# Optimization experiments

Measured on AMD Instinct MI355X. Metric: run time of the kernel, lower is better.

The kernel has to match this reference:

```python
import jax, jax.numpy as jnp
import numpy as np

INPUT_DIM = 2048
DIM = 1024
CODEBOOK_SIZE = 8192
COMMITMENT_COST = 0.25
N = 8192


def setup_inputs() -> dict:
    key = jax.random.key(0)
    ks = jax.random.split(key, 6)
    s_in = 1.0 / np.sqrt(INPUT_DIM)
    s_d = 1.0 / np.sqrt(DIM)
    return {
        "roi_feats": jax.random.normal(ks[0], (N, INPUT_DIM), dtype=jnp.float32),
        "W_in": jax.random.normal(ks[1], (DIM, INPUT_DIM), dtype=jnp.float32) * s_in,
        "b_in": jnp.zeros((DIM,), dtype=jnp.float32),
        "W_enc": jax.random.normal(ks[2], (DIM, DIM), dtype=jnp.float32) * s_d,
        "b_enc": jnp.zeros((DIM,), dtype=jnp.float32),
        "codebook": jax.random.uniform(ks[3], (CODEBOOK_SIZE, DIM), dtype=jnp.float32,
                                        minval=-1.0 / CODEBOOK_SIZE, maxval=1.0 / CODEBOOK_SIZE),
        "W_dec": jax.random.normal(ks[4], (DIM, DIM), dtype=jnp.float32) * s_d,
        "b_dec": jnp.zeros((DIM,), dtype=jnp.float32),
        "W_out": jax.random.normal(ks[5], (INPUT_DIM, DIM), dtype=jnp.float32) * s_d,
        "b_out": jnp.zeros((INPUT_DIM,), dtype=jnp.float32),
    }


def reference(roi_feats, W_in, b_in, W_enc, b_enc, codebook, W_dec, b_dec, W_out, b_out):
    # encoder(input_projection(x))
    z_e = (roi_feats @ W_in.T + b_in) @ W_enc.T + b_enc  # [N, DIM]
    # squared-euclidean distances to codebook: [N, K]
    d = (jnp.sum(z_e * z_e, axis=1, keepdims=True)
         - 2.0 * (z_e @ codebook.T)
         + jnp.sum(codebook * codebook, axis=1))
    ids = jnp.argmin(d, axis=-1)  # [N]
    z_q_raw = codebook[ids]  # [N, DIM]
    # straight-through estimator
    z_q = z_e + jax.lax.stop_gradient(z_q_raw - z_e)
    recon = (z_q @ W_dec.T + b_dec) @ W_out.T + b_out  # [N, INPUT_DIM]
    recon_loss = jnp.mean((recon - roi_feats) ** 2)
    embedding_loss = jnp.mean((jax.lax.stop_gradient(z_q) - z_e) ** 2)
    commitment_loss = jnp.mean((z_q - jax.lax.stop_gradient(z_e)) ** 2)
    vq_loss = recon_loss + embedding_loss + COMMITMENT_COST * commitment_loss
    return ids, z_q, recon, vq_loss, recon_loss, embedding_loss, commitment_loss
```

## Files before the change

kernel.cpp:

```cpp
#include <hip/hip_runtime.h>
#include <float.h>


#define N_ROWS 8192
#define IN_DIM 2048
#define DIM 1024
#define CBK 8192

#define PANEL_MASK_K1024_C32 0x0000000000401000ULL
#define PANEL_MASK_K2048_C32 0x0101001001001000ULL

#define SCREEN_DELTA 1.2e-3f

typedef __attribute__((ext_vector_type(8))) short short8;
typedef __attribute__((ext_vector_type(8))) unsigned short ushort8;
typedef __attribute__((ext_vector_type(4))) float f32x4;

__device__ __forceinline__ float sqf(float v) { return __builtin_fmaf(v, v, 0.0f); }

__device__ __forceinline__ unsigned short f2bf(float f) {
  unsigned int u = __float_as_uint(f);
  u += 0x7fffu + ((u >> 16) & 1u);
  return (unsigned short)(u >> 16);
}

__device__ __forceinline__ unsigned packsplit(float x) {
  const unsigned u = __float_as_uint(x);
  const unsigned hb = u & 0xFFFF0000u;
  const float rem = x - __uint_as_float(hb);
  return (u >> 16) | (__float_as_uint(rem) & 0xFFFF0000u);
}

__device__ __forceinline__ int swz128(int c) {
  return (c & 3) | (((c >> 3) & 7) << 2) | (((c >> 2) & 1) << 5) | ((c >> 6) << 6);
}

__device__ __forceinline__ float block_reduce_sum(float v) {
  __shared__ float sh[4];
  #pragma unroll
  for (int off = 32; off > 0; off >>= 1) v += __shfl_down(v, off, 64);
  const int lane = threadIdx.x & 63, w = threadIdx.x >> 6;
  if (lane == 0) sh[w] = v;
  __syncthreads();
  float r = 0.f;
  if (threadIdx.x == 0) r = sh[0] + sh[1] + sh[2] + sh[3];
  return r;
}

__device__ __forceinline__ float chain_d(const float* __restrict__ zsh,
                                         const float* __restrict__ cbr,
                                         float z2r, float c2e) {
  float part = 0.f;
  for (int k = 0; k < 384; ++k) part = __builtin_fmaf(zsh[k], cbr[k], part);
  float total = part;
  part = 0.f;
  for (int k = 384; k < 704; ++k) part = __builtin_fmaf(zsh[k], cbr[k], part);
  total = total + part;
  part = 0.f;
  for (int k = 704; k < 1024; ++k) part = __builtin_fmaf(zsh[k], cbr[k], part);
  total = total + part;
  return __builtin_fmaf(-2.0f, total, z2r) + c2e;
}

template <bool BT>
__global__ __launch_bounds__(256) void gemm128(
    const float* __restrict__ A, const float* __restrict__ B,
    const float* __restrict__ bias, float* __restrict__ C,
    int M, int N, int K) {
  __shared__ float As[2][16][132];
  __shared__ float Bs[2][16][132];
  const int tid = threadIdx.x;
  const int tx = tid & 15, ty = tid >> 4;
  const int bm = blockIdx.y, bn = blockIdx.x;

  const int mload = tid & 127, kh = tid >> 7;
  const size_t arow = (size_t)(bm * 128 + mload) * (size_t)K;
  const size_t brow = BT ? (size_t)(bn * 128 + mload) * (size_t)K : 0;
  const int swn = swz128(mload);
  const int c4 = (tid & 31) << 2;
  const int kr = tid >> 5;
  const int swc = swz128(c4);

  float acc[8][8];
  #pragma unroll
  for (int r = 0; r < 8; ++r)
    #pragma unroll
    for (int c = 0; c < 8; ++c) acc[r][c] = 0.f;

  const int boff = ((tx & 7) << 2) | ((tx >> 3) << 6);

  float4 av0, av1, bv0, bv1;
  av0 = *(const float4*)&A[arow + kh * 8];
  av1 = *(const float4*)&A[arow + kh * 8 + 4];
  if (BT) {
    bv0 = *(const float4*)&B[brow + kh * 8];
    bv1 = *(const float4*)&B[brow + kh * 8 + 4];
  } else {
    bv0 = *(const float4*)&B[(size_t)kr * N + bn * 128 + c4];
    bv1 = *(const float4*)&B[(size_t)(kr + 8) * N + bn * 128 + c4];
  }
  As[0][kh * 8 + 0][mload] = av0.x; As[0][kh * 8 + 1][mload] = av0.y;
  As[0][kh * 8 + 2][mload] = av0.z; As[0][kh * 8 + 3][mload] = av0.w;
  As[0][kh * 8 + 4][mload] = av1.x; As[0][kh * 8 + 5][mload] = av1.y;
  As[0][kh * 8 + 6][mload] = av1.z; As[0][kh * 8 + 7][mload] = av1.w;
  if (BT) {
    Bs[0][kh * 8 + 0][swn] = bv0.x; Bs[0][kh * 8 + 1][swn] = bv0.y;
    Bs[0][kh * 8 + 2][swn] = bv0.z; Bs[0][kh * 8 + 3][swn] = bv0.w;
    Bs[0][kh * 8 + 4][swn] = bv1.x; Bs[0][kh * 8 + 5][swn] = bv1.y;
    Bs[0][kh * 8 + 6][swn] = bv1.z; Bs[0][kh * 8 + 7][swn] = bv1.w;
  } else {
    *(float4*)&Bs[0][kr][swc] = bv0;
    *(float4*)&Bs[0][kr + 8][swc] = bv1;
  }
  const int nk = K >> 4;
  if (nk > 1) {
    av0 = *(const float4*)&A[arow + 16 + kh * 8];
    av1 = *(const float4*)&A[arow + 16 + kh * 8 + 4];
    if (BT) {
      bv0 = *(const float4*)&B[brow + 16 + kh * 8];
      bv1 = *(const float4*)&B[brow + 16 + kh * 8 + 4];
    } else {
      bv0 = *(const float4*)&B[(size_t)(16 + kr) * N + bn * 128 + c4];
      bv1 = *(const float4*)&B[(size_t)(16 + kr + 8) * N + bn * 128 + c4];
    }
  }
  __syncthreads();

  for (int ki = 0; ki < nk; ++ki) {
    const int p = ki & 1;
    if (ki + 1 < nk) {
      As[p ^ 1][kh * 8 + 0][mload] = av0.x; As[p ^ 1][kh * 8 + 1][mload] = av0.y;
      As[p ^ 1][kh * 8 + 2][mload] = av0.z; As[p ^ 1][kh * 8 + 3][mload] = av0.w;
      As[p ^ 1][kh * 8 + 4][mload] = av1.x; As[p ^ 1][kh * 8 + 5][mload] = av1.y;
      As[p ^ 1][kh * 8 + 6][mload] = av1.z; As[p ^ 1][kh * 8 + 7][mload] = av1.w;
      if (BT) {
        Bs[p ^ 1][kh * 8 + 0][swn] = bv0.x; Bs[p ^ 1][kh * 8 + 1][swn] = bv0.y;
        Bs[p ^ 1][kh * 8 + 2][swn] = bv0.z; Bs[p ^ 1][kh * 8 + 3][swn] = bv0.w;
        Bs[p ^ 1][kh * 8 + 4][swn] = bv1.x; Bs[p ^ 1][kh * 8 + 5][swn] = bv1.y;
        Bs[p ^ 1][kh * 8 + 6][swn] = bv1.z; Bs[p ^ 1][kh * 8 + 7][swn] = bv1.w;
      } else {
        *(float4*)&Bs[p ^ 1][kr][swc] = bv0;
        *(float4*)&Bs[p ^ 1][kr + 8][swc] = bv1;
      }
      if (ki + 2 < nk) {
        const int k2 = (ki + 2) << 4;
        av0 = *(const float4*)&A[arow + k2 + kh * 8];
        av1 = *(const float4*)&A[arow + k2 + kh * 8 + 4];
        if (BT) {
          bv0 = *(const float4*)&B[brow + k2 + kh * 8];
          bv1 = *(const float4*)&B[brow + k2 + kh * 8 + 4];
        } else {
          bv0 = *(const float4*)&B[(size_t)(k2 + kr) * N + bn * 128 + c4];
          bv1 = *(const float4*)&B[(size_t)(k2 + kr + 8) * N + bn * 128 + c4];
        }
      }
    }
    #pragma unroll
    for (int kk = 0; kk < 16; ++kk) {
      const float4 a0 = *(const float4*)&As[p][kk][ty * 8];
      const float4 a1 = *(const float4*)&As[p][kk][ty * 8 + 4];
      const float4 b0 = *(const float4*)&Bs[p][kk][boff];
      const float4 b1 = *(const float4*)&Bs[p][kk][boff + 32];
      const float ar[8] = {a0.x, a0.y, a0.z, a0.w, a1.x, a1.y, a1.z, a1.w};
      const float br[8] = {b0.x, b0.y, b0.z, b0.w, b1.x, b1.y, b1.z, b1.w};
      #pragma unroll
      for (int r = 0; r < 8; ++r)
        #pragma unroll
        for (int c = 0; c < 8; ++c) acc[r][c] = fmaf(ar[r], br[c], acc[r][c]);
    }
    __syncthreads();
  }

  const int gcol = bn * 128 + tx * 8;
  float bb[8] = {0, 0, 0, 0, 0, 0, 0, 0};
  if (bias) {
    const float4 v0 = *(const float4*)&bias[gcol];
    const float4 v1 = *(const float4*)&bias[gcol + 4];
    bb[0] = v0.x; bb[1] = v0.y; bb[2] = v0.z; bb[3] = v0.w;
    bb[4] = v1.x; bb[5] = v1.y; bb[6] = v1.z; bb[7] = v1.w;
  }
  #pragma unroll
  for (int r = 0; r < 8; ++r) {
    float* cp = &C[(size_t)(bm * 128 + ty * 8 + r) * N + gcol];
    float4 o0, o1;
    o0.x = acc[r][0] + bb[0]; o0.y = acc[r][1] + bb[1];
    o0.z = acc[r][2] + bb[2]; o0.w = acc[r][3] + bb[3];
    o1.x = acc[r][4] + bb[4]; o1.y = acc[r][5] + bb[5];
    o1.z = acc[r][6] + bb[6]; o1.w = acc[r][7] + bb[7];
    *(float4*)cp = o0;
    *(float4*)(cp + 4) = o1;
  }
}

__global__ __launch_bounds__(256) void emul_gemm_kernel(
    const float* __restrict__ A, const float* __restrict__ B,
    const float* __restrict__ bias, float* __restrict__ C,
    unsigned* __restrict__ ZP,
    int N, int K, int lda, int ldb, unsigned long long panel_mask) {
  __shared__ float As_[2][32][128];
  __shared__ float Bs_[2][32][128];
  const int tid = threadIdx.x;
  const int tx = tid & 15, ty = tid >> 4;
  const int row0 = blockIdx.y * 128, col0 = blockIdx.x * 128;
  const int sr = tid & 127, sh = tid >> 7;
  const int scol = (((sr >> 2) & 1) << 6) + ((sr >> 3) << 2) + (sr & 3);

  float part[8][8], total[8][8];
  #pragma unroll
  for (int r = 0; r < 8; ++r)
    #pragma unroll
    for (int e = 0; e < 8; ++e) { part[r][e] = 0.f; total[r][e] = 0.f; }

  float4 av[4], bv[4];
  #pragma unroll
  for (int q = 0; q < 4; ++q) {
    av[q] = *(const float4*)&A[(size_t)(row0 + sr) * lda + sh * 16 + q * 4];
    bv[q] = *(const float4*)&B[(size_t)(col0 + sr) * ldb + sh * 16 + q * 4];
  }
  #pragma unroll
  for (int q = 0; q < 4; ++q) {
    As_[0][sh * 16 + q * 4 + 0][sr] = av[q].x;
    As_[0][sh * 16 + q * 4 + 1][sr] = av[q].y;
    As_[0][sh * 16 + q * 4 + 2][sr] = av[q].z;
    As_[0][sh * 16 + q * 4 + 3][sr] = av[q].w;
    Bs_[0][sh * 16 + q * 4 + 0][scol] = bv[q].x;
    Bs_[0][sh * 16 + q * 4 + 1][scol] = bv[q].y;
    Bs_[0][sh * 16 + q * 4 + 2][scol] = bv[q].z;
    Bs_[0][sh * 16 + q * 4 + 3][scol] = bv[q].w;
  }
  const int nch = K >> 5;
  if (nch > 1) {
    #pragma unroll
    for (int q = 0; q < 4; ++q) {
      av[q] = *(const float4*)&A[(size_t)(row0 + sr) * lda + 32 + sh * 16 + q * 4];
      bv[q] = *(const float4*)&B[(size_t)(col0 + sr) * ldb + 32 + sh * 16 + q * 4];
    }
  }
  __syncthreads();

  for (int ci = 0; ci < nch; ++ci) {
    const int p = ci & 1;
    if (ci + 1 < nch) {
      #pragma unroll
      for (int q = 0; q < 4; ++q) {
        As_[p ^ 1][sh * 16 + q * 4 + 0][sr] = av[q].x;
        As_[p ^ 1][sh * 16 + q * 4 + 1][sr] = av[q].y;
        As_[p ^ 1][sh * 16 + q * 4 + 2][sr] = av[q].z;
        As_[p ^ 1][sh * 16 + q * 4 + 3][sr] = av[q].w;
        Bs_[p ^ 1][sh * 16 + q * 4 + 0][scol] = bv[q].x;
        Bs_[p ^ 1][sh * 16 + q * 4 + 1][scol] = bv[q].y;
        Bs_[p ^ 1][sh * 16 + q * 4 + 2][scol] = bv[q].z;
        Bs_[p ^ 1][sh * 16 + q * 4 + 3][scol] = bv[q].w;
      }
      if (ci + 2 < nch) {
        const int k2 = (ci + 2) << 5;
        #pragma unroll
        for (int q = 0; q < 4; ++q) {
          av[q] = *(const float4*)&A[(size_t)(row0 + sr) * lda + k2 + sh * 16 + q * 4];
          bv[q] = *(const float4*)&B[(size_t)(col0 + sr) * ldb + k2 + sh * 16 + q * 4];
        }
      }
    }
    if (ci && ((panel_mask >> ci) & 1ULL)) {
      #pragma unroll
      for (int r = 0; r < 8; ++r)
        #pragma unroll
        for (int e = 0; e < 8; ++e) { total[r][e] = total[r][e] + part[r][e]; part[r][e] = 0.f; }
    }
    #pragma unroll 4
    for (int kk = 0; kk < 32; ++kk) {
      const float4 za = *(const float4*)&As_[p][kk][ty * 8];
      const float4 zb = *(const float4*)&As_[p][kk][ty * 8 + 4];
      const float4 ca = *(const float4*)&Bs_[p][kk][tx * 4];
      const float4 cb4 = *(const float4*)&Bs_[p][kk][64 + tx * 4];
      const float zr[8] = {za.x, za.y, za.z, za.w, zb.x, zb.y, zb.z, zb.w};
      const float cr[8] = {ca.x, ca.y, ca.z, ca.w, cb4.x, cb4.y, cb4.z, cb4.w};
      #pragma unroll
      for (int r = 0; r < 8; ++r)
        #pragma unroll
        for (int e = 0; e < 8; ++e)
          part[r][e] = __builtin_fmaf(zr[r], cr[e], part[r][e]);
    }
    __syncthreads();
  }
  #pragma unroll
  for (int r = 0; r < 8; ++r)
    #pragma unroll
    for (int e = 0; e < 8; ++e) total[r][e] = total[r][e] + part[r][e];

  const float4 ba = *(const float4*)&bias[col0 + tx * 8];
  const float4 bb = *(const float4*)&bias[col0 + tx * 8 + 4];
  const float br8[8] = {ba.x, ba.y, ba.z, ba.w, bb.x, bb.y, bb.z, bb.w};
  #pragma unroll
  for (int r = 0; r < 8; ++r) {
    const size_t rowi = (size_t)(row0 + ty * 8 + r);
    float ov[8];
    #pragma unroll
    for (int j = 0; j < 8; ++j) ov[j] = total[r][j] + br8[j];
    float* cp = &C[rowi * N + col0 + tx * 8];
    float4 o0, o1;
    o0.x = ov[0]; o0.y = ov[1]; o0.z = ov[2]; o0.w = ov[3];
    o1.x = ov[4]; o1.y = ov[5]; o1.z = ov[6]; o1.w = ov[7];
    *(float4*)cp = o0;
    *(float4*)(cp + 4) = o1;
    if (ZP) {
      uint4 p0, p1;
      p0.x = packsplit(ov[0]); p0.y = packsplit(ov[1]);
      p0.z = packsplit(ov[2]); p0.w = packsplit(ov[3]);
      p1.x = packsplit(ov[4]); p1.y = packsplit(ov[5]);
      p1.z = packsplit(ov[6]); p1.w = packsplit(ov[7]);
      unsigned* zp = &ZP[rowi * N + col0 + tx * 8];
      *(uint4*)zp = p0;
      *(uint4*)(zp + 4) = p1;
    }
  }
}

__global__ __launch_bounds__(256) void mfma_screen_kernel(
    const unsigned* __restrict__ ZP, const float* __restrict__ CB,
    const float* __restrict__ Z2, const float* __restrict__ C2,
    uint4* __restrict__ recs) {
  __shared__ unsigned short Zs[128 * 64];
  __shared__ unsigned short Cs[128 * 64];
  __shared__ int rowminI[128];
  __shared__ int cnt[128];
  __shared__ unsigned short cand[128][12];
  const int tid = threadIdx.x;
  const int wid = tid >> 6, lane = tid & 63;
  const int e0 = blockIdx.x * 128, row0 = blockIdx.y * 128;
  const int wr = (wid >> 1) * 64, wc = (wid & 1) * 64;

  if (tid < 128) { rowminI[tid] = 0x7F800000; cnt[tid] = 0; }

  f32x4 acc[4][4];
  #pragma unroll
  for (int m = 0; m < 4; ++m)
    #pragma unroll
    for (int n = 0; n < 4; ++n)
      #pragma unroll
      for (int j = 0; j < 4; ++j) acc[m][n][j] = 0.f;

  const int stg_r = tid >> 3, stg_kg = (tid & 7) * 4;

  for (int k0 = 0; k0 < 1024; k0 += 32) {
    __syncthreads();
    #pragma unroll
    for (int s = 0; s < 4; ++s) {
      const int r = stg_r + s * 32;
      const int swz = (r & 7) << 4;
      const int bhi = (r * 128 + stg_kg * 2) ^ swz;
      const int blo = (r * 128 + 64 + stg_kg * 2) ^ swz;
      const uint4 p = *(const uint4*)&ZP[(size_t)(row0 + r) * 1024 + k0 + stg_kg];
      uint2 zh, zl;
      zh.x = (p.x & 0xFFFFu) | (p.y << 16);
      zh.y = (p.z & 0xFFFFu) | (p.w << 16);
      zl.x = (p.x >> 16) | (p.y & 0xFFFF0000u);
      zl.y = (p.z >> 16) | (p.w & 0xFFFF0000u);
      *(uint2*)((char*)Zs + bhi) = zh;
      *(uint2*)((char*)Zs + blo) = zl;
      const float4 cv = *(const float4*)&CB[(size_t)(e0 + r) * 1024 + k0 + stg_kg];
      const float cf[4] = {cv.x, cv.y, cv.z, cv.w};
      unsigned ch[4], cl[4];
      #pragma unroll
      for (int i = 0; i < 4; ++i) {
        const unsigned u = __float_as_uint(cf[i]);
        ch[i] = u & 0xFFFF0000u;
        const float rem = cf[i] - __uint_as_float(ch[i]);
        cl[i] = __float_as_uint(rem) & 0xFFFF0000u;
      }
      uint2 cph, cpl;
      cph.x = (ch[0] >> 16) | ch[1];
      cph.y = (ch[2] >> 16) | ch[3];
      cpl.x = (cl[0] >> 16) | cl[1];
      cpl.y = (cl[2] >> 16) | cl[3];
      *(uint2*)((char*)Cs + bhi) = cph;
      *(uint2*)((char*)Cs + blo) = cpl;
    }
    __syncthreads();
    const int kb2 = 16 * (lane >> 4);
    short8 ah[4], al[4], bh[4], bl[4];
    #pragma unroll
    for (int m = 0; m < 4; ++m) {
      const int r = wr + m * 16 + (lane & 15);
      const int swz = (r & 7) << 4;
      ah[m] = *(const short8*)((const char*)Zs + ((r * 128 + kb2) ^ swz));
      al[m] = *(const short8*)((const char*)Zs + ((r * 128 + 64 + kb2) ^ swz));
    }
    #pragma unroll
    for (int n = 0; n < 4; ++n) {
      const int r = wc + n * 16 + (lane & 15);
      const int swz = (r & 7) << 4;
      bh[n] = *(const short8*)((const char*)Cs + ((r * 128 + kb2) ^ swz));
      bl[n] = *(const short8*)((const char*)Cs + ((r * 128 + 64 + kb2) ^ swz));
    }
    #pragma unroll
    for (int m = 0; m < 4; ++m)
      #pragma unroll
      for (int n = 0; n < 4; ++n) {
        acc[m][n] = __builtin_amdgcn_mfma_f32_16x16x32_bf16(ah[m], bh[n], acc[m][n], 0, 0, 0);
        acc[m][n] = __builtin_amdgcn_mfma_f32_16x16x32_bf16(ah[m], bl[n], acc[m][n], 0, 0, 0);
        acc[m][n] = __builtin_amdgcn_mfma_f32_16x16x32_bf16(al[m], bh[n], acc[m][n], 0, 0, 0);
      }
  }

  float dv[4][4][4];
  #pragma unroll
  for (int m = 0; m < 4; ++m)
    #pragma unroll
    for (int j = 0; j < 4; ++j) {
      const int rg = row0 + wr + m * 16 + (lane >> 4) * 4 + j;
      const float z2r = Z2[rg];
      float lm = FLT_MAX;
      #pragma unroll
      for (int n = 0; n < 4; ++n) {
        const float d = __builtin_fmaf(-2.0f, acc[m][n][j], z2r) +
                        C2[e0 + wc + n * 16 + (lane & 15)];
        dv[m][n][j] = d;
        lm = fminf(lm, d);
      }
      #pragma unroll
      for (int msk = 1; msk < 16; msk <<= 1)
        lm = fminf(lm, __shfl_xor(lm, msk, 64));
      if ((lane & 15) == 0)
        atomicMin(&rowminI[wr + m * 16 + (lane >> 4) * 4 + j], __float_as_int(lm));
    }
  __syncthreads();
  #pragma unroll
  for (int m = 0; m < 4; ++m)
    #pragma unroll
    for (int j = 0; j < 4; ++j) {
      const int rl = wr + m * 16 + (lane >> 4) * 4 + j;
      const float thr = __int_as_float(rowminI[rl]) + SCREEN_DELTA;
      #pragma unroll
      for (int n = 0; n < 4; ++n) {
        if (dv[m][n][j] <= thr) {
          const int pos = atomicAdd(&cnt[rl], 1);
          if (pos < 12)
            cand[rl][pos] = (unsigned short)(e0 + wc + n * 16 + (lane & 15));
        }
      }
    }
  __syncthreads();
  if (tid < 128) {
    uint4 a, b;
    a.x = (unsigned)rowminI[tid];
    a.y = (unsigned)cnt[tid];
    a.z = (unsigned)cand[tid][0] | ((unsigned)cand[tid][1] << 16);
    a.w = (unsigned)cand[tid][2] | ((unsigned)cand[tid][3] << 16);
    b.x = (unsigned)cand[tid][4] | ((unsigned)cand[tid][5] << 16);
    b.y = (unsigned)cand[tid][6] | ((unsigned)cand[tid][7] << 16);
    b.z = (unsigned)cand[tid][8] | ((unsigned)cand[tid][9] << 16);
    b.w = (unsigned)cand[tid][10] | ((unsigned)cand[tid][11] << 16);
    const size_t base = ((size_t)(row0 + tid) * 64 + blockIdx.x) * 2;
    recs[base] = a;
    recs[base + 1] = b;
  }
}

__global__ __launch_bounds__(256) void collect_rescore_kernel(
    const uint4* __restrict__ recs, const float* __restrict__ Z,
    const float* __restrict__ CB, const float* __restrict__ Z2,
    const float* __restrict__ C2, int* __restrict__ ids,
    float* __restrict__ o_ids, float* __restrict__ o_zq,
    float* __restrict__ esum) {
  __shared__ float zsh[1024];
  __shared__ float gmin_sh;
  __shared__ int lcnt, ovf, ewin;
  __shared__ unsigned short list[64];
  __shared__ unsigned long long kred[4];
  const int row = blockIdx.x, tid = threadIdx.x;
  if (tid == 0) { lcnt = 0; ovf = 0; }
  uint4 r0 = make_uint4(0, 0, 0, 0), r1 = make_uint4(0, 0, 0, 0);
  float mymin = FLT_MAX;
  if (tid < 64) {
    const size_t base = ((size_t)row * 64 + tid) * 2;
    r0 = recs[base];
    r1 = recs[base + 1];
    mymin = __uint_as_float(r0.x);
  }
  for (int i = tid; i < 1024; i += 256) zsh[i] = Z[(size_t)row * 1024 + i];
  if (tid < 64) {
    float m = mymin;
    #pragma unroll
    for (int off = 32; off > 0; off >>= 1) m = fminf(m, __shfl_down(m, off, 64));
    if (tid == 0) gmin_sh = m;
  }
  __syncthreads();
  const float thr = gmin_sh + SCREEN_DELTA;
  if (tid < 64 && mymin <= thr) {
    const int c = (int)r0.y;
    if (c > 12) {
      atomicOr(&ovf, 1);
    } else {
      unsigned short idxs[12];
      idxs[0] = r0.z & 0xFFFF; idxs[1] = r0.z >> 16;
      idxs[2] = r0.w & 0xFFFF; idxs[3] = r0.w >> 16;
      idxs[4] = r1.x & 0xFFFF; idxs[5] = r1.x >> 16;
      idxs[6] = r1.y & 0xFFFF; idxs[7] = r1.y >> 16;
      idxs[8] = r1.z & 0xFFFF; idxs[9] = r1.z >> 16;
      idxs[10] = r1.w & 0xFFFF; idxs[11] = r1.w >> 16;
      for (int i = 0; i < c; ++i) {
        const int pos = atomicAdd(&lcnt, 1);
        if (pos < 64) list[pos] = idxs[i];
        else atomicOr(&ovf, 1);
      }
    }
  }
  __syncthreads();
  const float z2r = Z2[row];
  unsigned long long key = ~0ULL;
  if (ovf) {
    for (int e = tid; e < CBK; e += 256) {
      const float d = chain_d(zsh, &CB[(size_t)e * 1024], z2r, C2[e]);
      const unsigned long long k =
          ((unsigned long long)__float_as_uint(d) << 32) | (unsigned)e;
      key = (k < key) ? k : key;
    }
  } else {
    const int n = lcnt < 64 ? lcnt : 64;
    if (tid < n) {
      const int e = list[tid];
      const float d = chain_d(zsh, &CB[(size_t)e * 1024], z2r, C2[e]);
      key = ((unsigned long long)__float_as_uint(d) << 32) | (unsigned)e;
    }
  }
  #pragma unroll
  for (int off = 32; off > 0; off >>= 1) {
    const unsigned long long o = __shfl_down(key, off, 64);
    key = (o < key) ? o : key;
  }
  if ((tid & 63) == 0) kred[tid >> 6] = key;
  __syncthreads();
  if (tid == 0) {
    unsigned long long k = kred[0];
    k = (kred[1] < k) ? kred[1] : k;
    k = (kred[2] < k) ? kred[2] : k;
    k = (kred[3] < k) ? kred[3] : k;
    const int e = (int)(k & 0xFFFFFFFFu);
    ids[row] = e;
    o_ids[row] = (float)e;
    ewin = e;
  }
  __syncthreads();
  const int e2 = ewin;
  float s = 0.f;
  for (int i = tid; i < 1024; i += 256) {
    const float c = CB[(size_t)e2 * 1024 + i];
    o_zq[(size_t)row * 1024 + i] = c;
    const float d = zsh[i] - c;
    s = __builtin_fmaf(d, d, s);
  }
  const float r2 = block_reduce_sum(s);
  if (tid == 0) esum[row] = r2;
}

__global__ __launch_bounds__(256) void mfma_recon_kernel(
    const float* __restrict__ A, const float* __restrict__ B,
    const float* __restrict__ bias, float* __restrict__ C) {
  __shared__ unsigned short Abf[128 * 64];
  __shared__ unsigned short Bbf[128 * 64];
  const int tid = threadIdx.x;
  const int wid = tid >> 6, lane = tid & 63;
  const int row0 = blockIdx.y * 128, col0 = blockIdx.x * 128;
  const int wr = (wid >> 1) * 64, wc = (wid & 1) * 64;

  f32x4 acc[4][4];
  #pragma unroll
  for (int m = 0; m < 4; ++m)
    #pragma unroll
    for (int n = 0; n < 4; ++n)
      #pragma unroll
      for (int j = 0; j < 4; ++j) acc[m][n][j] = 0.f;

  for (int k0 = 0; k0 < 1024; k0 += 64) {
    __syncthreads();
    #pragma unroll
    for (int q = 0; q < 4; ++q) {
      const int g = tid + q * 256;
      const int r = g >> 3;
      const int kg = (g & 7) * 8;
      const float4 a0 = *(const float4*)&A[(size_t)(row0 + r) * 1024 + k0 + kg];
      const float4 a1 = *(const float4*)&A[(size_t)(row0 + r) * 1024 + k0 + kg + 4];
      const float4 b0 = *(const float4*)&B[(size_t)(col0 + r) * 1024 + k0 + kg];
      const float4 b1 = *(const float4*)&B[(size_t)(col0 + r) * 1024 + k0 + kg + 4];
      ushort8 pa, pb;
      pa[0] = f2bf(a0.x); pa[1] = f2bf(a0.y); pa[2] = f2bf(a0.z); pa[3] = f2bf(a0.w);
      pa[4] = f2bf(a1.x); pa[5] = f2bf(a1.y); pa[6] = f2bf(a1.z); pa[7] = f2bf(a1.w);
      pb[0] = f2bf(b0.x); pb[1] = f2bf(b0.y); pb[2] = f2bf(b0.z); pb[3] = f2bf(b0.w);
      pb[4] = f2bf(b1.x); pb[5] = f2bf(b1.y); pb[6] = f2bf(b1.z); pb[7] = f2bf(b1.w);
      const int byte = (r * 128 + kg * 2) ^ ((r & 7) << 4);
      *(ushort8*)((char*)Abf + byte) = pa;
      *(ushort8*)((char*)Bbf + byte) = pb;
    }
    __syncthreads();
    #pragma unroll
    for (int kh = 0; kh < 2; ++kh) {
      const int kb = kh * 32 + 8 * (lane >> 4);
      short8 afr[4], bfr[4];
      #pragma unroll
      for (int m = 0; m < 4; ++m) {
        const int r = wr + m * 16 + (lane & 15);
        const int byte = (r * 128 + kb * 2) ^ ((r & 7) << 4);
        afr[m] = *(const short8*)((const char*)Abf + byte);
      }
      #pragma unroll
      for (int n = 0; n < 4; ++n) {
        const int r = wc + n * 16 + (lane & 15);
        const int byte = (r * 128 + kb * 2) ^ ((r & 7) << 4);
        bfr[n] = *(const short8*)((const char*)Bbf + byte);
      }
      #pragma unroll
      for (int m = 0; m < 4; ++m)
        #pragma unroll
        for (int n = 0; n < 4; ++n)
          acc[m][n] = __builtin_amdgcn_mfma_f32_16x16x32_bf16(
              afr[m], bfr[n], acc[m][n], 0, 0, 0);
    }
  }

  #pragma unroll
  for (int m = 0; m < 4; ++m)
    #pragma unroll
    for (int n = 0; n < 4; ++n) {
      const int col = col0 + wc + n * 16 + (lane & 15);
      const float bc = bias[col];
      #pragma unroll
      for (int j = 0; j < 4; ++j) {
        const int row = row0 + wr + m * 16 + (lane >> 4) * 4 + j;
        C[(size_t)row * 2048 + col] = acc[m][n][j] + bc;
      }
    }
}

__global__ __launch_bounds__(256) void sumsq1024_kernel(
    const float* __restrict__ X, float* __restrict__ out) {
  __shared__ float rows[4][1024];
  __shared__ float leaves[4][8];
  const int tid = threadIdx.x;
  const int row0 = blockIdx.x * 4;
  for (int i = tid; i < 4096; i += 256)
    rows[i >> 10][i & 1023] = X[(size_t)row0 * 1024 + i];
  __syncthreads();
  if (tid < 32) {
    const int r = tid >> 3, lf = tid & 7;
    const float* a = &rows[r][lf * 128];
    float s0 = sqf(a[0]), s1 = sqf(a[1]), s2 = sqf(a[2]), s3 = sqf(a[3]);
    float s4 = sqf(a[4]), s5 = sqf(a[5]), s6 = sqf(a[6]), s7 = sqf(a[7]);
    for (int i = 8; i < 128; i += 8) {
      s0 = s0 + sqf(a[i + 0]); s1 = s1 + sqf(a[i + 1]);
      s2 = s2 + sqf(a[i + 2]); s3 = s3 + sqf(a[i + 3]);
      s4 = s4 + sqf(a[i + 4]); s5 = s5 + sqf(a[i + 5]);
      s6 = s6 + sqf(a[i + 6]); s7 = s7 + sqf(a[i + 7]);
    }
    leaves[r][lf] = ((s0 + s1) + (s2 + s3)) + ((s4 + s5) + (s6 + s7));
  }
  __syncthreads();
  if (tid < 4) {
    const float* L = leaves[tid];
    const float p01 = L[0] + L[1], p23 = L[2] + L[3];
    const float p45 = L[4] + L[5], p67 = L[6] + L[7];
    out[row0 + tid] = ((p01 + p23) + (p45 + p67));
  }
}

__global__ __launch_bounds__(256) void rowdot_bias_kernel(
    const float* __restrict__ W, const float* __restrict__ v,
    const float* __restrict__ b2, float* __restrict__ out) {
  const int row = blockIdx.x;
  const float4 w4 = *(const float4*)&W[(size_t)row * 1024 + threadIdx.x * 4];
  const float4 v4 = *(const float4*)&v[threadIdx.x * 4];
  const float s = w4.x * v4.x + w4.y * v4.y + w4.z * v4.z + w4.w * v4.w;
  const float r = block_reduce_sum(s);
  if (threadIdx.x == 0) out[row] = r + b2[row];
}

__global__ __launch_bounds__(256) void sqdiff_partial_kernel(
    const float* __restrict__ a, const float* __restrict__ b,
    float* __restrict__ part) {
  const size_t base = (size_t)blockIdx.x * 2048 + (size_t)threadIdx.x * 8;
  const float4 x0 = *(const float4*)&a[base];
  const float4 x1 = *(const float4*)&a[base + 4];
  const float4 y0 = *(const float4*)&b[base];
  const float4 y1 = *(const float4*)&b[base + 4];
  float s = 0.f;
  float d;
  d = x0.x - y0.x; s += d * d; d = x0.y - y0.y; s += d * d;
  d = x0.z - y0.z; s += d * d; d = x0.w - y0.w; s += d * d;
  d = x1.x - y1.x; s += d * d; d = x1.y - y1.y; s += d * d;
  d = x1.z - y1.z; s += d * d; d = x1.w - y1.w; s += d * d;
  const float r = block_reduce_sum(s);
  if (threadIdx.x == 0) part[blockIdx.x] = r;
}

__global__ __launch_bounds__(256) void final_losses_kernel(
    const float* __restrict__ rp, const float* __restrict__ esum,
    float* __restrict__ o) {
  __shared__ double sh[4];
  const int lane = threadIdx.x & 63, w = threadIdx.x >> 6;
  double s = 0.0;
  for (int i = threadIdx.x; i < 8192; i += 256) s += (double)rp[i];
  #pragma unroll
  for (int off = 32; off > 0; off >>= 1) s += __shfl_down(s, off, 64);
  if (lane == 0) sh[w] = s;
  __syncthreads();
  double rl = 0.0;
  if (threadIdx.x == 0) rl = (sh[0] + sh[1] + sh[2] + sh[3]) / ((double)N_ROWS * IN_DIM);
  __syncthreads();
  double s2 = 0.0;
  for (int i = threadIdx.x; i < 8192; i += 256) s2 += (double)esum[i];
  #pragma unroll
  for (int off = 32; off > 0; off >>= 1) s2 += __shfl_down(s2, off, 64);
  if (lane == 0) sh[w] = s2;
  __syncthreads();
  if (threadIdx.x == 0) {
    const double el = (sh[0] + sh[1] + sh[2] + sh[3]) / ((double)N_ROWS * DIM);
    o[0] = (float)(rl + el + 0.25 * el);
    o[1] = (float)rl;
    o[2] = (float)el;
    o[3] = (float)el;
  }
}

extern "C" void kernel_launch(void* const* d_in, const int* in_sizes, int n_in,
                              void* d_out, int out_size, void* d_ws, size_t ws_size,
                              hipStream_t stream) {
  const float* roi   = (const float*)d_in[0];
  const float* W_in  = (const float*)d_in[1];
  const float* b_in  = (const float*)d_in[2];
  const float* W_enc = (const float*)d_in[3];
  const float* b_enc = (const float*)d_in[4];
  const float* cb    = (const float*)d_in[5];
  const float* W_dec = (const float*)d_in[6];
  const float* b_dec = (const float*)d_in[7];
  const float* W_out = (const float*)d_in[8];
  const float* b_out = (const float*)d_in[9];

  float* out = (float*)d_out;
  float* o_ids   = out;
  float* o_zq    = out + 8192;
  float* o_recon = out + 8192 + (size_t)N_ROWS * DIM;
  float* o_scal  = out + 8192 + (size_t)N_ROWS * DIM + (size_t)N_ROWS * IN_DIM;

  float*  ws    = (float*)d_ws;
  float*  W_dc  = ws;
  float*  z2    = ws + 2097152;
  float*  c2    = ws + 2105344;
  int*    ids   = (int*)(ws + 2113536);
  float*  b_dc  = ws + 2121728;
  float*  esum  = ws + 2123776;
  float*  rp    = ws + 2131968;

  float*    t     = o_recon;
  float*    z     = o_recon + (size_t)N_ROWS * DIM;
  uint4*    recs  = (uint4*)o_recon;
  unsigned* zpack = (unsigned*)o_zq;

  rowdot_bias_kernel<<<IN_DIM, 256, 0, stream>>>(W_out, b_dec, b_out, b_dc);
  gemm128<false><<<dim3(DIM / 128, IN_DIM / 128), 256, 0, stream>>>(
      W_out, W_dec, nullptr, W_dc, IN_DIM, DIM, DIM);

  emul_gemm_kernel<<<dim3(DIM / 128, N_ROWS / 128), 256, 0, stream>>>(
      roi, W_in, b_in, t, nullptr, DIM, IN_DIM, IN_DIM, IN_DIM,
      PANEL_MASK_K2048_C32);
  emul_gemm_kernel<<<dim3(DIM / 128, N_ROWS / 128), 256, 0, stream>>>(
      t, W_enc, b_enc, z, zpack, DIM, DIM, DIM, DIM, PANEL_MASK_K1024_C32);

  sumsq1024_kernel<<<N_ROWS / 4, 256, 0, stream>>>(z, z2);
  sumsq1024_kernel<<<CBK / 4, 256, 0, stream>>>(cb, c2);

  mfma_screen_kernel<<<dim3(CBK / 128, N_ROWS / 128), 256, 0, stream>>>(
      zpack, cb, z2, c2, recs);
  collect_rescore_kernel<<<N_ROWS, 256, 0, stream>>>(
      recs, z, cb, z2, c2, ids, o_ids, o_zq, esum);

  mfma_recon_kernel<<<dim3(IN_DIM / 128, N_ROWS / 128), 256, 0, stream>>>(
      o_zq, W_dc, b_dc, o_recon);

  sqdiff_partial_kernel<<<(N_ROWS * IN_DIM) / 2048, 256, 0, stream>>>(
      o_recon, roi, rp);
  final_losses_kernel<<<1, 256, 0, stream>>>(rp, esum, o_scal);
}
```

Baseline: 1.473 ms.

## Presplit codebook and z into separate hi/lo bf16 planes; shrink screen records

The codebook is split once into separate hi/lo bf16 arrays by a new kernel, and the encoder GEMM writes z as separate hi/lo planes. The screen kernel can then copy both straight into shared memory instead of re-splitting fp32 codebook values in every row block. Per-tile candidate records shrink from 12 slots in two uint4s to 4 slots in one uint4, stored in workspace. This cuts staging arithmetic and record traffic but adds a codebook pass, and rows with more than 4 candidates in a tile now fall back to the full rescore more often.

```diff
diff --git a/kernel.cpp b/kernel.cpp
--- a/kernel.cpp
+++ b/kernel.cpp
@@ -14,6 +14,7 @@
 
 typedef __attribute__((ext_vector_type(8))) short short8;
 typedef __attribute__((ext_vector_type(8))) unsigned short ushort8;
+typedef __attribute__((ext_vector_type(4))) unsigned short ushort4v;
 typedef __attribute__((ext_vector_type(4))) float f32x4;
 
 __device__ __forceinline__ float sqf(float v) { return __builtin_fmaf(v, v, 0.0f); }
@@ -22,13 +23,6 @@
   unsigned int u = __float_as_uint(f);
   u += 0x7fffu + ((u >> 16) & 1u);
   return (unsigned short)(u >> 16);
-}
-
-__device__ __forceinline__ unsigned packsplit(float x) {
-  const unsigned u = __float_as_uint(x);
-  const unsigned hb = u & 0xFFFF0000u;
-  const float rem = x - __uint_as_float(hb);
-  return (u >> 16) | (__float_as_uint(rem) & 0xFFFF0000u);
 }
 
 __device__ __forceinline__ int swz128(int c) {
@@ -195,7 +189,7 @@
 __global__ __launch_bounds__(256) void emul_gemm_kernel(
     const float* __restrict__ A, const float* __restrict__ B,
     const float* __restrict__ bias, float* __restrict__ C,
-    unsigned* __restrict__ ZP,
+    unsigned short* __restrict__ ZHI, unsigned short* __restrict__ ZLO,
     int N, int K, int lda, int ldb, unsigned long long panel_mask) {
   __shared__ float As_[2][32][128];
   __shared__ float Bs_[2][32][128];
@@ -303,28 +297,49 @@
     o1.x = ov[4]; o1.y = ov[5]; o1.z = ov[6]; o1.w = ov[7];
     *(float4*)cp = o0;
     *(float4*)(cp + 4) = o1;
-    if (ZP) {
-      uint4 p0, p1;
-      p0.x = packsplit(ov[0]); p0.y = packsplit(ov[1]);
-      p0.z = packsplit(ov[2]); p0.w = packsplit(ov[3]);
-      p1.x = packsplit(ov[4]); p1.y = packsplit(ov[5]);
-      p1.z = packsplit(ov[6]); p1.w = packsplit(ov[7]);
-      unsigned* zp = &ZP[rowi * N + col0 + tx * 8];
-      *(uint4*)zp = p0;
-      *(uint4*)(zp + 4) = p1;
-    }
-  }
+    if (ZHI) {
+      ushort8 hv, lv;
+      #pragma unroll
+      for (int j = 0; j < 8; ++j) {
+        const unsigned u = __float_as_uint(ov[j]);
+        hv[j] = (unsigned short)(u >> 16);
+        const float rem = ov[j] - __uint_as_float(u & 0xFFFF0000u);
+        lv[j] = (unsigned short)(__float_as_uint(rem) >> 16);
+      }
+      *(ushort8*)&ZHI[rowi * N + col0 + tx * 8] = hv;
+      *(ushort8*)&ZLO[rowi * N + col0 + tx * 8] = lv;
+    }
+  }
+}
+
+__global__ __launch_bounds__(256) void cbsplit_kernel(
+    const float* __restrict__ CB, unsigned short* __restrict__ CHI,
+    unsigned short* __restrict__ CLO) {
+  const size_t base = (size_t)blockIdx.x * 1024 + threadIdx.x * 4;
+  const float4 v = *(const float4*)&CB[base];
+  const float xf[4] = {v.x, v.y, v.z, v.w};
+  ushort4v hv, lv;
+  #pragma unroll
+  for (int i = 0; i < 4; ++i) {
+    const unsigned u = __float_as_uint(xf[i]);
+    hv[i] = (unsigned short)(u >> 16);
+    const float rem = xf[i] - __uint_as_float(u & 0xFFFF0000u);
+    lv[i] = (unsigned short)(__float_as_uint(rem) >> 16);
+  }
+  *(ushort4v*)&CHI[base] = hv;
+  *(ushort4v*)&CLO[base] = lv;
 }
 
 __global__ __launch_bounds__(256) void mfma_screen_kernel(
-    const unsigned* __restrict__ ZP, const float* __restrict__ CB,
+    const unsigned short* __restrict__ ZHI, const unsigned short* __restrict__ ZLO,
+    const unsigned short* __restrict__ CHI, const unsigned short* __restrict__ CLO,
     const float* __restrict__ Z2, const float* __restrict__ C2,
     uint4* __restrict__ recs) {
   __shared__ unsigned short Zs[128 * 64];
   __shared__ unsigned short Cs[128 * 64];
   __shared__ int rowminI[128];
   __shared__ int cnt[128];
-  __shared__ unsigned short cand[128][12];
+  __shared__ unsigned short cand[128][4];
   const int tid = threadIdx.x;
   const int wid = tid >> 6, lane = tid & 63;
   const int e0 = blockIdx.x * 128, row0 = blockIdx.y * 128;
@@ -350,31 +365,12 @@
       const int swz = (r & 7) << 4;
       const int bhi = (r * 128 + stg_kg * 2) ^ swz;
       const int blo = (r * 128 + 64 + stg_kg * 2) ^ swz;
-      const uint4 p = *(const uint4*)&ZP[(size_t)(row0 + r) * 1024 + k0 + stg_kg];
-      uint2 zh, zl;
-      zh.x = (p.x & 0xFFFFu) | (p.y << 16);
-      zh.y = (p.z & 0xFFFFu) | (p.w << 16);
-      zl.x = (p.x >> 16) | (p.y & 0xFFFF0000u);
-      zl.y = (p.z >> 16) | (p.w & 0xFFFF0000u);
-      *(uint2*)((char*)Zs + bhi) = zh;
-      *(uint2*)((char*)Zs + blo) = zl;
-      const float4 cv = *(const float4*)&CB[(size_t)(e0 + r) * 1024 + k0 + stg_kg];
-      const float cf[4] = {cv.x, cv.y, cv.z, cv.w};
-      unsigned ch[4], cl[4];
-      #pragma unroll
-      for (int i = 0; i < 4; ++i) {
-        const unsigned u = __float_as_uint(cf[i]);
-        ch[i] = u & 0xFFFF0000u;
-        const float rem = cf[i] - __uint_as_float(ch[i]);
-        cl[i] = __float_as_uint(rem) & 0xFFFF0000u;
-      }
-      uint2 cph, cpl;
-      cph.x = (ch[0] >> 16) | ch[1];
-      cph.y = (ch[2] >> 16) | ch[3];
-      cpl.x = (cl[0] >> 16) | cl[1];
-      cpl.y = (cl[2] >> 16) | cl[3];
-      *(uint2*)((char*)Cs + bhi) = cph;
-      *(uint2*)((char*)Cs + blo) = cpl;
+      const size_t zoff = (size_t)(row0 + r) * 1024 + k0 + stg_kg;
+      const size_t coff = (size_t)(e0 + r) * 1024 + k0 + stg_kg;
+      *(uint2*)((char*)Zs + bhi) = *(const uint2*)&ZHI[zoff];
+      *(uint2*)((char*)Zs + blo) = *(const uint2*)&ZLO[zoff];
+      *(uint2*)((char*)Cs + bhi) = *(const uint2*)&CHI[coff];
+      *(uint2*)((char*)Cs + blo) = *(const uint2*)&CLO[coff];
     }
     __syncthreads();
     const int kb2 = 16 * (lane >> 4);
@@ -435,25 +431,19 @@
       for (int n = 0; n < 4; ++n) {
         if (dv[m][n][j] <= thr) {
           const int pos = atomicAdd(&cnt[rl], 1);
-          if (pos < 12)
+          if (pos < 4)
             cand[rl][pos] = (unsigned short)(e0 + wc + n * 16 + (lane & 15));
         }
       }
     }
   __syncthreads();
   if (tid < 128) {
-    uint4 a, b;
+    uint4 a;
     a.x = (unsigned)rowminI[tid];
-    a.y = (unsigned)cnt[tid];
-    a.z = (unsigned)cand[tid][0] | ((unsigned)cand[tid][1] << 16);
-    a.w = (unsigned)cand[tid][2] | ((unsigned)cand[tid][3] << 16);
-    b.x = (unsigned)cand[tid][4] | ((unsigned)cand[tid][5] << 16);
-    b.y = (unsigned)cand[tid][6] | ((unsigned)cand[tid][7] << 16);
-    b.z = (unsigned)cand[tid][8] | ((unsigned)cand[tid][9] << 16);
-    b.w = (unsigned)cand[tid][10] | ((unsigned)cand[tid][11] << 16);
-    const size_t base = ((size_t)(row0 + tid) * 64 + blockIdx.x) * 2;
-    recs[base] = a;
-    recs[base + 1] = b;
+    a.y = (unsigned)cand[tid][0] | ((unsigned)cand[tid][1] << 16);
+    a.z = (unsigned)cand[tid][2] | ((unsigned)cand[tid][3] << 16);
+    a.w = (unsigned)cnt[tid];
+    recs[(size_t)(row0 + tid) * 64 + blockIdx.x] = a;
   }
 }
 
@@ -470,12 +460,10 @@
   __shared__ unsigned long long kred[4];
   const int row = blockIdx.x, tid = threadIdx.x;
   if (tid == 0) { lcnt = 0; ovf = 0; }
-  uint4 r0 = make_uint4(0, 0, 0, 0), r1 = make_uint4(0, 0, 0, 0);
+  uint4 r0 = make_uint4(0, 0, 0, 0);
   float mymin = FLT_MAX;
   if (tid < 64) {
-    const size_t base = ((size_t)row * 64 + tid) * 2;
-    r0 = recs[base];
-    r1 = recs[base + 1];
+    r0 = recs[(size_t)row * 64 + tid];
     mymin = __uint_as_float(r0.x);
   }
   for (int i = tid; i < 1024; i += 256) zsh[i] = Z[(size_t)row * 1024 + i];
@@ -488,17 +476,13 @@
   __syncthreads();
   const float thr = gmin_sh + SCREEN_DELTA;
   if (tid < 64 && mymin <= thr) {
-    const int c = (int)r0.y;
-    if (c > 12) {
+    const int c = (int)r0.w;
+    if (c > 4) {
       atomicOr(&ovf, 1);
     } else {
-      unsigned short idxs[12];
-      idxs[0] = r0.z & 0xFFFF; idxs[1] = r0.z >> 16;
-      idxs[2] = r0.w & 0xFFFF; idxs[3] = r0.w >> 16;
-      idxs[4] = r1.x & 0xFFFF; idxs[5] = r1.x >> 16;
-      idxs[6] = r1.y & 0xFFFF; idxs[7] = r1.y >> 16;
-      idxs[8] = r1.z & 0xFFFF; idxs[9] = r1.z >> 16;
-      idxs[10] = r1.w & 0xFFFF; idxs[11] = r1.w >> 16;
+      unsigned short idxs[4];
+      idxs[0] = r0.y & 0xFFFF; idxs[1] = r0.y >> 16;
+      idxs[2] = r0.z & 0xFFFF; idxs[3] = r0.z >> 16;
       for (int i = 0; i < c; ++i) {
         const int pos = atomicAdd(&lcnt, 1);
         if (pos < 64) list[pos] = idxs[i];
@@ -748,28 +732,33 @@
   int*    ids   = (int*)(ws + 2113536);
   float*  b_dc  = ws + 2121728;
   float*  esum  = ws + 2123776;
+  uint4*  recs  = (uint4*)(ws + 2131968);
   float*  rp    = ws + 2131968;
 
-  float*    t     = o_recon;
-  float*    z     = o_recon + (size_t)N_ROWS * DIM;
-  uint4*    recs  = (uint4*)o_recon;
-  unsigned* zpack = (unsigned*)o_zq;
+  float*          t    = o_recon;
+  float*          z    = o_recon + (size_t)N_ROWS * DIM;
+  unsigned short* cbhi = (unsigned short*)o_recon;
+  unsigned short* cblo = cbhi + (size_t)CBK * DIM;
+  unsigned short* zhi  = (unsigned short*)o_zq;
+  unsigned short* zlo  = zhi + (size_t)N_ROWS * DIM;
 
   rowdot_bias_kernel<<<IN_DIM, 256, 0, stream>>>(W_out, b_dec, b_out, b_dc);
   gemm128<false><<<dim3(DIM / 128, IN_DIM / 128), 256, 0, stream>>>(
       W_out, W_dec, nullptr, W_dc, IN_DIM, DIM, DIM);
 
   emul_gemm_kernel<<<dim3(DIM / 128, N_ROWS / 128), 256, 0, stream>>>(
-      roi, W_in, b_in, t, nullptr, DIM, IN_DIM, IN_DIM, IN_DIM,
+      roi, W_in, b_in, t, nullptr, nullptr, DIM, IN_DIM, IN_DIM, IN_DIM,
       PANEL_MASK_K2048_C32);
   emul_gemm_kernel<<<dim3(DIM / 128, N_ROWS / 128), 256, 0, stream>>>(
-      t, W_enc, b_enc, z, zpack, DIM, DIM, DIM, DIM, PANEL_MASK_K1024_C32);
+      t, W_enc, b_enc, z, zhi, zlo, DIM, DIM, DIM, DIM, PANEL_MASK_K1024_C32);
 
   sumsq1024_kernel<<<N_ROWS / 4, 256, 0, stream>>>(z, z2);
   sumsq1024_kernel<<<CBK / 4, 256, 0, stream>>>(cb, c2);
 
+  cbsplit_kernel<<<CBK, 256, 0, stream>>>(cb, cbhi, cblo);
+
   mfma_screen_kernel<<<dim3(CBK / 128, N_ROWS / 128), 256, 0, stream>>>(
-      zpack, cb, z2, c2, recs);
+      zhi, zlo, cbhi, cblo, z2, c2, recs);
   collect_rescore_kernel<<<N_ROWS, 256, 0, stream>>>(
       recs, z, cb, z2, c2, ids, o_ids, o_zq, esum);
 
```

Result: no change. 1.481 ms (+0.5%).
